# Kernel optimization log

Hardware: AMD Instinct MI355X
Metric: run time of the kernel (lower is better)

The kernel has to match this reference:

```python
import jax, jax.numpy as jnp
import numpy as np

D_MODEL, H, D_K, D_V, D_FF = 1024, 16, 64, 64, 4096
B, L = 2, 2048
EPS = 1e-5


def layer_norm(x, g, b):
    mu = jnp.mean(x, axis=-1, keepdims=True)
    var = jnp.mean(jnp.square(x - mu), axis=-1, keepdims=True)
    return (x - mu) * jax.lax.rsqrt(var + EPS) * g + b


def setup_inputs() -> dict:
    key = jax.random.key(0)
    ks = jax.random.split(key, 12)
    s = 0.02
    x = jax.random.normal(ks[0], (B, L, D_MODEL), dtype=jnp.float32)
    Wq = jax.random.normal(ks[1], (H, D_MODEL, D_K), dtype=jnp.float32) * s
    Wk = jax.random.normal(ks[2], (H, D_MODEL, D_K), dtype=jnp.float32) * s
    Wv = jax.random.normal(ks[3], (H, D_MODEL, D_V), dtype=jnp.float32) * s
    bq = jnp.zeros((H, D_K), dtype=jnp.float32)
    bk = jnp.zeros((H, D_K), dtype=jnp.float32)
    bv = jnp.zeros((H, D_V), dtype=jnp.float32)
    Wo = jax.random.normal(ks[4], (H * D_V, D_MODEL), dtype=jnp.float32) * s
    W1 = jax.random.normal(ks[5], (D_MODEL, D_FF), dtype=jnp.float32) * s
    b1 = jnp.zeros((D_FF,), dtype=jnp.float32)
    W2 = jax.random.normal(ks[6], (D_FF, D_MODEL), dtype=jnp.float32) * s
    ln1_g = jnp.ones((D_MODEL,), dtype=jnp.float32)
    ln1_b = jnp.zeros((D_MODEL,), dtype=jnp.float32)
    ln2_g = jnp.ones((D_MODEL,), dtype=jnp.float32)
    ln2_b = jnp.zeros((D_MODEL,), dtype=jnp.float32)
    return dict(x=x, Wq=Wq, bq=bq, Wk=Wk, bk=bk, Wv=Wv, bv=bv, Wo=Wo,
                ln1_g=ln1_g, ln1_b=ln1_b, W1=W1, b1=b1, W2=W2,
                ln2_g=ln2_g, ln2_b=ln2_b)


def reference(x, Wq, bq, Wk, bk, Wv, bv, Wo, ln1_g, ln1_b, W1, b1, W2, ln2_g, ln2_b):
    # Batched multi-head attention (all heads at once, equivalent to the
    # per-head Python loop in the original module).
    Q = jnp.einsum('bld,hdk->bhlk', x, Wq) + bq[None, :, None, :]
    K = jnp.einsum('bld,hdk->bhlk', x, Wk) + bk[None, :, None, :]
    V = jnp.einsum('bld,hdv->bhlv', x, Wv) + bv[None, :, None, :]
    scores = jnp.einsum('bhlk,bhmk->bhlm', Q, K) * (1.0 / jnp.sqrt(jnp.float32(D_K)))
    attn = jax.nn.softmax(scores, axis=-1)
    O = jnp.einsum('bhlm,bhmv->bhlv', attn, V)        # [b,h,l,dv]
    O = jnp.transpose(O, (0, 2, 1, 3)).reshape(x.shape[0], x.shape[1], H * D_V)
    mha = O @ Wo                                       # [b,l,d_model]
    # residual + LayerNorm (dropout_prob=0 -> identity)
    h1 = layer_norm(x + mha, ln1_g, ln1_b)
    ff = jax.nn.relu(h1 @ W1 + b1) @ W2
    return layer_norm(h1 + ff, ln2_g, ln2_b)
```

## Files before the change

kernel.cpp:

```cpp
#include <hip/hip_runtime.h>

typedef unsigned short u16;
typedef unsigned int u32;
typedef short bf16x8 __attribute__((ext_vector_type(8)));
typedef float f32x4 __attribute__((ext_vector_type(4)));
typedef unsigned int u32x2 __attribute__((ext_vector_type(2)));

#define D_MODEL 1024
#define NH 16
#define DK 64
#define DFF 4096
#define BATCH 2
#define SEQ 2048
#define BL (BATCH*SEQ)
#define NQKV 3072
#define Q_SCALE 0.18033688011f

__device__ __forceinline__ float bfraw2f(u16 u) {
    union { u32 i; float f; } c; c.i = ((u32)u) << 16; return c.f;
}
__device__ __forceinline__ u16 f2bfraw(float f) {
    union { float f; u32 i; } c; c.f = f;
    u32 i = c.i;
    u32 lsb = (i >> 16) & 1u;
    i += 0x7fffu + lsb;
    return (u16)(i >> 16);
}
__device__ __forceinline__ u32 fasu(float f) {
    union { float f; u32 i; } c; c.f = f; return c.i;
}
__device__ __forceinline__ u32 pack_bf2(float lo, float hi) {
    return __builtin_amdgcn_perm(fasu(hi) + 0x8000u, fasu(lo) + 0x8000u,
                                 0x07060302u);
}
__device__ __forceinline__ void gload_lds16(const u16* g, u16* l) {
    __builtin_amdgcn_global_load_lds(
        (const __attribute__((address_space(1))) void*)g,
        (__attribute__((address_space(3))) void*)l, 16, 0, 0);
}

__global__ __launch_bounds__(256) void cast_f32_bf16(const float* __restrict__ in,
                                                     u16* __restrict__ out) {
    int i = (blockIdx.x * 256 + threadIdx.x) * 4;
    f32x4 v = *(const f32x4*)&in[i];
#pragma unroll
    for (int j = 0; j < 4; j++) out[i + j] = f2bfraw(v[j]);
}


__global__ __launch_bounds__(256) void transpose2d(const float* __restrict__ in,
                                                   u16* __restrict__ out,
                                                   int R, int C) {
    __shared__ u16 t[64][65];
    int c0 = blockIdx.x * 64, r0 = blockIdx.y * 64;
    int col = threadIdx.x & 63, rr = threadIdx.x >> 6;
    for (int i = rr; i < 64; i += 4)
        t[i][col] = f2bfraw(in[(size_t)(r0 + i) * C + c0 + col]);
    __syncthreads();
    for (int i = rr; i < 64; i += 4)
        out[(size_t)(c0 + i) * R + r0 + col] = t[col][i];
}

__global__ __launch_bounds__(256) void transpose_wqkv(const float* __restrict__ Wq,
                                                      const float* __restrict__ Wk,
                                                      const float* __restrict__ Wv,
                                                      u16* __restrict__ out) {
    __shared__ u16 t[64][65];
    int d0 = blockIdx.x * 64;
    int h = blockIdx.y;
    int ms = blockIdx.z;
    const float* W = (ms == 0) ? Wq : (ms == 1) ? Wk : Wv;
    const float* src = W + (size_t)h * D_MODEL * DK;
    int col = threadIdx.x & 63, rr = threadIdx.x >> 6;
    for (int i = rr; i < 64; i += 4)
        t[i][col] = f2bfraw(src[(size_t)(d0 + i) * DK + col]);
    __syncthreads();
    u16* dst = out + (size_t)(ms * 1024 + h * 64) * D_MODEL;
    for (int i = rr; i < 64; i += 4)
        dst[(size_t)i * D_MODEL + d0 + col] = t[col][i];
}

__global__ __launch_bounds__(256) void concat_bias(const float* __restrict__ bq,
                                                   const float* __restrict__ bk,
                                                   const float* __restrict__ bv,
                                                   float* __restrict__ out) {
    int i = blockIdx.x * 256 + threadIdx.x;
    out[i] = (i < 1024) ? bq[i] : (i < 2048) ? bk[i - 1024] : bv[i - 2048];
}


template <int OUT_F32, int RELU, int HASBIAS, int SPLITK, int SCALEQ, int VSTORE>
__global__ __launch_bounds__(256, 4) void gemm_bt(const u16* __restrict__ A,
                                                  const u16* __restrict__ Bt,
                                                  const float* __restrict__ bias,
                                                  void* __restrict__ Cout,
                                                  u16* __restrict__ vtout,
                                                  int M, int N, int K) {
    __shared__ __attribute__((aligned(16))) u16 As[128 * 64];
    __shared__ __attribute__((aligned(16))) u16 Bs[128 * 64];
    const int tid = threadIdx.x;
    const int lane = tid & 63, wid = tid >> 6;
    const int quad = lane >> 4, l16 = lane & 15;
    const int m0 = blockIdx.x * 128, n0 = blockIdx.y * 128;
    const int z = (SPLITK > 1) ? blockIdx.z : 0;
    const int Klen = K / SPLITK;
    const int kend = (z + 1) * Klen;
    const int wm = (wid >> 1) * 64, wn = (wid & 1) * 64;

    f32x4 acc[4][4];
#pragma unroll
    for (int i = 0; i < 4; i++)
#pragma unroll
        for (int j = 0; j < 4; j++) acc[i][j] = (f32x4){0.f, 0.f, 0.f, 0.f};

    const int srow = lane >> 3, scol = (lane & 7) * 8;

    for (int kb = z * Klen; kb < kend; kb += 64) {
#pragma unroll
        for (int p = 0; p < 4; p++) {
            int c = wid * 4 + p;
            int row = c * 8 + srow;
            gload_lds16(&A[(size_t)(m0 + row) * K + kb + scol], &As[c * 512]);
            gload_lds16(&Bt[(size_t)(n0 + row) * K + kb + scol], &Bs[c * 512]);
        }
        __syncthreads();
#pragma unroll
        for (int kh = 0; kh < 2; kh++) {
            bf16x8 af[4], bf[4];
#pragma unroll
            for (int t = 0; t < 4; t++) {
                af[t] = *(const bf16x8*)&As[(wm + t * 16 + l16) * 64 + kh * 32 + quad * 8];
                bf[t] = *(const bf16x8*)&Bs[(wn + t * 16 + l16) * 64 + kh * 32 + quad * 8];
            }
#pragma unroll
            for (int i = 0; i < 4; i++)
#pragma unroll
                for (int j = 0; j < 4; j++)
                    acc[i][j] = __builtin_amdgcn_mfma_f32_16x16x32_bf16(
                        af[i], bf[j], acc[i][j], 0, 0, 0);
        }
        __syncthreads();
    }

    if (VSTORE && n0 >= 2048) {
#pragma unroll
        for (int i = 0; i < 4; i++) {
            int row0 = m0 + wm + i * 16 + quad * 4;
            int bb = row0 >> 11, l = row0 & 2047;
#pragma unroll
            for (int j = 0; j < 4; j++) {
                int col = n0 + wn + j * 16 + l16;
                float bv = HASBIAS ? bias[col] : 0.f;
                int dv = col - 2048;
                u32x2 w;
                w.x = pack_bf2(acc[i][j][0] + bv, acc[i][j][1] + bv);
                w.y = pack_bf2(acc[i][j][2] + bv, acc[i][j][3] + bv);
                *(u32x2*)&vtout[((size_t)(bb * 1024 + dv)) * 2048 + l] = w;
            }
        }
        return;
    }

    float* outf = (float*)Cout + (size_t)z * M * N;
#pragma unroll
    for (int i = 0; i < 4; i++) {
#pragma unroll
        for (int j = 0; j < 4; j++) {
#pragma unroll
            for (int r = 0; r < 4; r++) {
                int row = m0 + wm + i * 16 + quad * 4 + r;
                int col = n0 + wn + j * 16 + l16;
                float v = acc[i][j][r];
                if (HASBIAS) v += bias[col];
                if (RELU) v = v > 0.f ? v : 0.f;
                if (SCALEQ && col < 1024) v *= Q_SCALE;
                if (OUT_F32)
                    outf[(size_t)row * N + col] = v;
                else
                    ((u16*)Cout)[(size_t)row * N + col] = f2bfraw(v);
            }
        }
    }
}

__global__ __launch_bounds__(256, 2) void attn_kernel(const u16* __restrict__ qkv,
                                                      const u16* __restrict__ vt,
                                                      u16* __restrict__ O) {
    constexpr int LDK = 72;
    constexpr int LDV = 136;
    constexpr int LDP = 136;
    __shared__ __attribute__((aligned(16))) u16 Ks[128 * LDK];
    __shared__ __attribute__((aligned(16))) u16 Vs[64 * LDV];
    __shared__ __attribute__((aligned(16))) u16 Ps[4][32 * LDP];

    const int tid = threadIdx.x;
    const int lane = tid & 63, wid = tid >> 6;
    const int quad = lane >> 4, l16 = lane & 15;
    const int b = blockIdx.z, h = blockIdx.y;
    const int q0 = blockIdx.x * 128 + wid * 32;

    bf16x8 qf[2][2];
#pragma unroll
    for (int qt = 0; qt < 2; qt++) {
        const size_t qrow = (size_t)(b * SEQ + q0 + qt * 16 + l16) * NQKV + h * DK;
        qf[qt][0] = *(const bf16x8*)&qkv[qrow + quad * 8];
        qf[qt][1] = *(const bf16x8*)&qkv[qrow + 32 + quad * 8];
    }
    const u16* Kbase = qkv + (size_t)(b * SEQ) * NQKV + D_MODEL + h * DK;
    const u16* Vbase = vt + (size_t)((b * NH + h) * DK) * SEQ;

    f32x4 oacc[4][2];
#pragma unroll
    for (int d = 0; d < 4; d++) {
        oacc[d][0] = (f32x4){0.f, 0.f, 0.f, 0.f};
        oacc[d][1] = (f32x4){0.f, 0.f, 0.f, 0.f};
    }
    float lr[2] = {0.f, 0.f};
    const f32x4 Z = {0.f, 0.f, 0.f, 0.f};

    for (int kt = 0; kt < SEQ; kt += 128) {
        bf16x8 kreg[4], vreg[4];
#pragma unroll
        for (int p = 0; p < 4; p++) {
            int s = p * 256 + tid;
            kreg[p] = *(const bf16x8*)&Kbase[(size_t)(kt + (s >> 3)) * NQKV + (s & 7) * 8];
            vreg[p] = *(const bf16x8*)&Vbase[(size_t)(s >> 4) * SEQ + kt + (s & 15) * 8];
        }
#pragma unroll
        for (int p = 0; p < 4; p++) {
            int s = p * 256 + tid;
            *(bf16x8*)&Ks[(s >> 3) * LDK + (s & 7) * 8] = kreg[p];
            *(bf16x8*)&Vs[(s >> 4) * LDV + (s & 15) * 8] = vreg[p];
        }
        __syncthreads();

        f32x4 sacc[8][2];
#pragma unroll
        for (int nt = 0; nt < 8; nt++) {
            const u16* kr = &Ks[(nt * 16 + l16) * LDK];
            bf16x8 kf0 = *(const bf16x8*)&kr[quad * 8];
            bf16x8 kf1 = *(const bf16x8*)&kr[32 + quad * 8];
#pragma unroll
            for (int qt = 0; qt < 2; qt++) {
                f32x4 s0 = __builtin_amdgcn_mfma_f32_16x16x32_bf16(kf0, qf[qt][0], Z, 0, 0, 0);
                sacc[nt][qt] = __builtin_amdgcn_mfma_f32_16x16x32_bf16(kf1, qf[qt][1], s0, 0, 0, 0);
            }
        }

#pragma unroll
        for (int qt = 0; qt < 2; qt++) {
            u16* prow = &Ps[wid][(qt * 16 + l16) * LDP];
#pragma unroll
            for (int nt = 0; nt < 8; nt++) {
                float p0 = __builtin_amdgcn_exp2f(sacc[nt][qt][0]);
                float p1 = __builtin_amdgcn_exp2f(sacc[nt][qt][1]);
                float p2 = __builtin_amdgcn_exp2f(sacc[nt][qt][2]);
                float p3 = __builtin_amdgcn_exp2f(sacc[nt][qt][3]);
                lr[qt] += (p0 + p1) + (p2 + p3);
                u32x2 w;
                w.x = pack_bf2(p0, p1);
                w.y = pack_bf2(p2, p3);
                *(u32x2*)&prow[nt * 16 + quad * 4] = w;
            }
        }

#pragma unroll
        for (int ks = 0; ks < 4; ks++) {
            bf16x8 pf0 = *(const bf16x8*)&Ps[wid][l16 * LDP + ks * 32 + quad * 8];
            bf16x8 pf1 = *(const bf16x8*)&Ps[wid][(16 + l16) * LDP + ks * 32 + quad * 8];
#pragma unroll
            for (int d = 0; d < 4; d++) {
                bf16x8 vf = *(const bf16x8*)&Vs[(d * 16 + l16) * LDV + ks * 32 + quad * 8];
                oacc[d][0] = __builtin_amdgcn_mfma_f32_16x16x32_bf16(vf, pf0, oacc[d][0], 0, 0, 0);
                oacc[d][1] = __builtin_amdgcn_mfma_f32_16x16x32_bf16(vf, pf1, oacc[d][1], 0, 0, 0);
            }
        }
        __syncthreads();
    }

#pragma unroll
    for (int qt = 0; qt < 2; qt++) {
        lr[qt] += __shfl_xor(lr[qt], 16, 64);
        lr[qt] += __shfl_xor(lr[qt], 32, 64);
    }

#pragma unroll
    for (int qt = 0; qt < 2; qt++) {
        float iv = 1.f / lr[qt];
        size_t row = (size_t)(b * SEQ + q0 + qt * 16 + l16);
#pragma unroll
        for (int d = 0; d < 4; d++) {
            float o0 = oacc[d][qt][0] * iv, o1 = oacc[d][qt][1] * iv;
            float o2 = oacc[d][qt][2] * iv, o3 = oacc[d][qt][3] * iv;
            u32x2 w;
            w.x = ((u32)f2bfraw(o1) << 16) | f2bfraw(o0);
            w.y = ((u32)f2bfraw(o3) << 16) | f2bfraw(o2);
            *(u32x2*)&O[row * D_MODEL + h * DK + d * 16 + quad * 4] = w;
        }
    }
}

__global__ __launch_bounds__(256) void ln3_kernel(const float* __restrict__ xa,
                                                  const float* __restrict__ xb,
                                                  const float* __restrict__ xc,
                                                  const float* __restrict__ g,
                                                  const float* __restrict__ be,
                                                  u16* __restrict__ out_bf,
                                                  float* __restrict__ out_f) {
    int row = blockIdx.x;
    int tid = threadIdx.x;
    const float* pa = xa + (size_t)row * D_MODEL;
    const float* pb = xb + (size_t)row * D_MODEL;
    const float* pc = xc + (size_t)row * D_MODEL;
    int c = tid * 4;
    f32x4 av = *(const f32x4*)&pa[c];
    f32x4 bv = *(const f32x4*)&pb[c];
    f32x4 cv = *(const f32x4*)&pc[c];
    float v[4];
    float s = 0.f, ss = 0.f;
#pragma unroll
    for (int i = 0; i < 4; i++) {
        v[i] = av[i] + bv[i] + cv[i];
        s += v[i];
        ss += v[i] * v[i];
    }
#pragma unroll
    for (int off = 32; off; off >>= 1) {
        s += __shfl_down(s, off, 64);
        ss += __shfl_down(ss, off, 64);
    }
    __shared__ float red[8];
    int wid = tid >> 6, lane = tid & 63;
    if (lane == 0) { red[wid] = s; red[4 + wid] = ss; }
    __syncthreads();
    if (tid == 0) {
        red[0] = red[0] + red[1] + red[2] + red[3];
        red[4] = red[4] + red[5] + red[6] + red[7];
    }
    __syncthreads();
    float mu = red[0] * (1.f / D_MODEL);
    float var = red[4] * (1.f / D_MODEL) - mu * mu;
    float rs = rsqrtf(var + 1e-5f);
#pragma unroll
    for (int i = 0; i < 4; i++) {
        float o = (v[i] - mu) * rs * g[c + i] + be[c + i];
        if (out_f) out_f[(size_t)row * D_MODEL + c + i] = o;
        if (out_bf) out_bf[(size_t)row * D_MODEL + c + i] = f2bfraw(o);
    }
}

extern "C" void kernel_launch(void* const* d_in, const int* in_sizes, int n_in,
                              void* d_out, int out_size, void* d_ws, size_t ws_size,
                              hipStream_t stream) {
    const float* x   = (const float*)d_in[0];
    const float* Wq  = (const float*)d_in[1];
    const float* bq  = (const float*)d_in[2];
    const float* Wk  = (const float*)d_in[3];
    const float* bk  = (const float*)d_in[4];
    const float* Wv  = (const float*)d_in[5];
    const float* bv  = (const float*)d_in[6];
    const float* Wo  = (const float*)d_in[7];
    const float* g1  = (const float*)d_in[8];
    const float* be1 = (const float*)d_in[9];
    const float* W1  = (const float*)d_in[10];
    const float* b1  = (const float*)d_in[11];
    const float* W2  = (const float*)d_in[12];
    const float* g2  = (const float*)d_in[13];
    const float* be2 = (const float*)d_in[14];

    char* w = (char*)d_ws;
    auto alloc = [&](size_t bytes) {
        char* p = w;
        w += (bytes + 255) & ~(size_t)255;
        return p;
    };
    u16* wqkv_t = (u16*)alloc((size_t)NQKV * D_MODEL * 2);
    u16* wo_t   = (u16*)alloc((size_t)D_MODEL * D_MODEL * 2);
    u16* w1_t   = (u16*)alloc((size_t)DFF * D_MODEL * 2);
    u16* w2_t   = (u16*)alloc((size_t)D_MODEL * DFF * 2);
    float* bqkv = (float*)alloc((size_t)NQKV * 4);
    u16* x_bf   = (u16*)alloc((size_t)BL * D_MODEL * 2);
    u16* qkvbuf = (u16*)alloc((size_t)BL * NQKV * 2);
    u16* vtbuf  = (u16*)alloc((size_t)BATCH * NH * DK * SEQ * 2);
    u16* obuf   = (u16*)alloc((size_t)BL * D_MODEL * 2);
    float* mha_p = (float*)alloc((size_t)2 * BL * D_MODEL * 4);
    u16* h1_bf  = (u16*)alloc((size_t)BL * D_MODEL * 2);
    float* h1_f = (float*)alloc((size_t)BL * D_MODEL * 4);
    u16* ffa    = (u16*)alloc((size_t)BL * DFF * 2);
    float* ffb_p = (float*)alloc((size_t)2 * BL * D_MODEL * 4);

    cast_f32_bf16<<<dim3(BL * D_MODEL / 1024), 256, 0, stream>>>(x, x_bf);
    transpose_wqkv<<<dim3(16, 16, 3), 256, 0, stream>>>(Wq, Wk, Wv, wqkv_t);
    transpose2d<<<dim3(16, 16), 256, 0, stream>>>(Wo, wo_t, 1024, 1024);
    transpose2d<<<dim3(64, 16), 256, 0, stream>>>(W1, w1_t, 1024, 4096);
    transpose2d<<<dim3(16, 64), 256, 0, stream>>>(W2, w2_t, 4096, 1024);
    concat_bias<<<dim3(12), 256, 0, stream>>>(bq, bk, bv, bqkv);

    gemm_bt<0, 0, 1, 1, 1, 1><<<dim3(32, 24), 256, 0, stream>>>(
        x_bf, wqkv_t, bqkv, qkvbuf, vtbuf, BL, NQKV, D_MODEL);
    attn_kernel<<<dim3(16, 16, 2), 256, 0, stream>>>(qkvbuf, vtbuf, obuf);
    gemm_bt<1, 0, 0, 2, 0, 0><<<dim3(32, 8, 2), 256, 0, stream>>>(
        obuf, wo_t, nullptr, mha_p, nullptr, BL, D_MODEL, D_MODEL);
    ln3_kernel<<<dim3(BL), 256, 0, stream>>>(x, mha_p, mha_p + (size_t)BL * D_MODEL,
                                             g1, be1, h1_bf, h1_f);
    gemm_bt<0, 1, 1, 1, 0, 0><<<dim3(32, 32), 256, 0, stream>>>(
        h1_bf, w1_t, b1, ffa, nullptr, BL, DFF, D_MODEL);
    gemm_bt<1, 0, 0, 2, 0, 0><<<dim3(32, 8, 2), 256, 0, stream>>>(
        ffa, w2_t, nullptr, ffb_p, nullptr, BL, D_MODEL, DFF);
    ln3_kernel<<<dim3(BL), 256, 0, stream>>>(h1_f, ffb_p, ffb_p + (size_t)BL * D_MODEL,
                                             g2, be2, nullptr, (float*)d_out);
}
```

Measured before the change: 377.8 us.

## Prefetch next K/V tile into registers, XOR-swizzle LDS, raise MFMA priority

Result: no change. 373.4 us (-1.2%).

```diff
diff --git a/kernel.cpp b/kernel.cpp
--- a/kernel.cpp
+++ b/kernel.cpp
@@ -186,16 +186,14 @@
 __global__ __launch_bounds__(256, 2) void attn_kernel(const u16* __restrict__ qkv,
                                                       const u16* __restrict__ vt,
                                                       u16* __restrict__ O) {
-    constexpr int LDK = 72;
-    constexpr int LDV = 136;
-    constexpr int LDP = 136;
-    __shared__ __attribute__((aligned(16))) u16 Ks[128 * LDK];
-    __shared__ __attribute__((aligned(16))) u16 Vs[64 * LDV];
-    __shared__ __attribute__((aligned(16))) u16 Ps[4][32 * LDP];
+    __shared__ __attribute__((aligned(16))) u16 Ks[128 * 64];
+    __shared__ __attribute__((aligned(16))) u16 Vs[64 * 128];
+    __shared__ __attribute__((aligned(16))) u16 Ps[4][32 * 128];
 
     const int tid = threadIdx.x;
     const int lane = tid & 63, wid = tid >> 6;
     const int quad = lane >> 4, l16 = lane & 15;
+    const int sw = l16 & 7;
     const int b = blockIdx.z, h = blockIdx.y;
     const int q0 = blockIdx.x * 128 + wid * 32;
 
@@ -218,38 +216,48 @@
     float lr[2] = {0.f, 0.f};
     const f32x4 Z = {0.f, 0.f, 0.f, 0.f};
 
-    for (int kt = 0; kt < SEQ; kt += 128) {
-        bf16x8 kreg[4], vreg[4];
+    bf16x8 kreg[4], vreg[4];
+    auto stage_load = [&](int kt2) {
 #pragma unroll
         for (int p = 0; p < 4; p++) {
             int s = p * 256 + tid;
-            kreg[p] = *(const bf16x8*)&Kbase[(size_t)(kt + (s >> 3)) * NQKV + (s & 7) * 8];
-            vreg[p] = *(const bf16x8*)&Vbase[(size_t)(s >> 4) * SEQ + kt + (s & 15) * 8];
-        }
+            kreg[p] = *(const bf16x8*)&Kbase[(size_t)(kt2 + (s >> 3)) * NQKV + (s & 7) * 8];
+            vreg[p] = *(const bf16x8*)&Vbase[(size_t)(s >> 4) * SEQ + kt2 + (s & 15) * 8];
+        }
+    };
+    stage_load(0);
+
+    for (int kt = 0; kt < SEQ; kt += 128) {
 #pragma unroll
         for (int p = 0; p < 4; p++) {
             int s = p * 256 + tid;
-            *(bf16x8*)&Ks[(s >> 3) * LDK + (s & 7) * 8] = kreg[p];
-            *(bf16x8*)&Vs[(s >> 4) * LDV + (s & 15) * 8] = vreg[p];
+            int kr = s >> 3, kc = s & 7;
+            *(bf16x8*)&Ks[kr * 64 + ((kc ^ (kr & 7)) * 8)] = kreg[p];
+            int vr = s >> 4, vc = s & 15;
+            *(bf16x8*)&Vs[vr * 128 + ((vc ^ (vr & 7)) * 8)] = vreg[p];
         }
         __syncthreads();
 
+        if (kt + 128 < SEQ) stage_load(kt + 128);
+
         f32x4 sacc[8][2];
+        __builtin_amdgcn_s_setprio(1);
 #pragma unroll
         for (int nt = 0; nt < 8; nt++) {
-            const u16* kr = &Ks[(nt * 16 + l16) * LDK];
-            bf16x8 kf0 = *(const bf16x8*)&kr[quad * 8];
-            bf16x8 kf1 = *(const bf16x8*)&kr[32 + quad * 8];
+            const u16* krow = &Ks[(nt * 16 + l16) * 64];
+            bf16x8 kf0 = *(const bf16x8*)&krow[(quad ^ sw) * 8];
+            bf16x8 kf1 = *(const bf16x8*)&krow[((4 + quad) ^ sw) * 8];
 #pragma unroll
             for (int qt = 0; qt < 2; qt++) {
                 f32x4 s0 = __builtin_amdgcn_mfma_f32_16x16x32_bf16(kf0, qf[qt][0], Z, 0, 0, 0);
                 sacc[nt][qt] = __builtin_amdgcn_mfma_f32_16x16x32_bf16(kf1, qf[qt][1], s0, 0, 0, 0);
             }
         }
+        __builtin_amdgcn_s_setprio(0);
 
 #pragma unroll
         for (int qt = 0; qt < 2; qt++) {
-            u16* prow = &Ps[wid][(qt * 16 + l16) * LDP];
+            u16* prow = &Ps[wid][(qt * 16 + l16) * 128];
 #pragma unroll
             for (int nt = 0; nt < 8; nt++) {
                 float p0 = __builtin_amdgcn_exp2f(sacc[nt][qt][0]);
@@ -260,21 +268,25 @@
                 u32x2 w;
                 w.x = pack_bf2(p0, p1);
                 w.y = pack_bf2(p2, p3);
-                *(u32x2*)&prow[nt * 16 + quad * 4] = w;
-            }
-        }
-
+                int c = nt * 2 + (quad >> 1);
+                *(u32x2*)&prow[((c ^ sw) * 8) + (quad & 1) * 4] = w;
+            }
+        }
+
+        __builtin_amdgcn_s_setprio(1);
 #pragma unroll
         for (int ks = 0; ks < 4; ks++) {
-            bf16x8 pf0 = *(const bf16x8*)&Ps[wid][l16 * LDP + ks * 32 + quad * 8];
-            bf16x8 pf1 = *(const bf16x8*)&Ps[wid][(16 + l16) * LDP + ks * 32 + quad * 8];
+            int c = ks * 4 + quad;
+            bf16x8 pf0 = *(const bf16x8*)&Ps[wid][l16 * 128 + ((c ^ sw) * 8)];
+            bf16x8 pf1 = *(const bf16x8*)&Ps[wid][(16 + l16) * 128 + ((c ^ sw) * 8)];
 #pragma unroll
             for (int d = 0; d < 4; d++) {
-                bf16x8 vf = *(const bf16x8*)&Vs[(d * 16 + l16) * LDV + ks * 32 + quad * 8];
+                bf16x8 vf = *(const bf16x8*)&Vs[(d * 16 + l16) * 128 + ((c ^ sw) * 8)];
                 oacc[d][0] = __builtin_amdgcn_mfma_f32_16x16x32_bf16(vf, pf0, oacc[d][0], 0, 0, 0);
                 oacc[d][1] = __builtin_amdgcn_mfma_f32_16x16x32_bf16(vf, pf1, oacc[d][1], 0, 0, 0);
             }
         }
+        __builtin_amdgcn_s_setprio(0);
         __syncthreads();
     }
 
```
